# Optimization experiments

Measured on AMD Instinct MI355X. Metric: run time of the kernel, lower is better.

The kernel has to match this reference:

```python
import jax, jax.numpy as jnp
import numpy as np

N = 100000
E = 1600000
NEG_SLOPE = 0.2

def _gat_layer(x, src, dst, W, a_s, a_d, b, n):
    # GATConv (heads=1): h = xW; alpha_ij = softmax_i(leaky_relu(a_s.h_j + a_d.h_i))
    h = x @ W                                   # [N, F]
    s_src = h @ a_s                             # [N]
    s_dst = h @ a_d                             # [N]
    logits = jax.nn.leaky_relu(s_src[src] + s_dst[dst], NEG_SLOPE)  # [E]
    m = jax.ops.segment_max(logits, dst, num_segments=n)
    m = jnp.where(jnp.isfinite(m), m, 0.0)
    w = jnp.exp(logits - m[dst])
    denom = jax.ops.segment_sum(w, dst, num_segments=n)
    alpha = w / (denom[dst] + 1e-16)            # neighbor softmax per target node
    out = jax.ops.segment_sum(alpha[:, None] * h[src], dst, num_segments=n)
    return out + b

def setup_inputs() -> dict:
    key = jax.random.key(0)
    ks = jax.random.split(key, 12)
    def glorot(k, shape):
        fan = shape[0] + shape[-1] if len(shape) > 1 else shape[0]
        return jax.random.normal(k, shape, jnp.float32) * jnp.sqrt(2.0 / fan)
    x = jax.random.normal(ks[0], (N, 128), jnp.float32)
    edge_index = jax.random.randint(ks[1], (2, E), 0, N, dtype=jnp.int32)
    return {
        'x': x, 'edge_index': edge_index,
        'W1': glorot(ks[2], (128, 64)), 'a1s': glorot(ks[3], (64,)), 'a1d': glorot(ks[4], (64,)), 'b1': jnp.zeros((64,), jnp.float32),
        'W2': glorot(ks[5], (64, 64)), 'a2s': glorot(ks[6], (64,)), 'a2d': glorot(ks[7], (64,)), 'b2': jnp.zeros((64,), jnp.float32),
        'W3': glorot(ks[8], (64, 32)), 'a3s': glorot(ks[9], (32,)), 'a3d': glorot(ks[10], (32,)), 'b3': jnp.zeros((32,), jnp.float32),
    }

def reference(x, edge_index, W1, a1s, a1d, b1, W2, a2s, a2d, b2, W3, a3s, a3d, b3):
    n = x.shape[0]
    # PyG GATConv adds self-loops by default
    loops = jnp.arange(n, dtype=edge_index.dtype)
    src = jnp.concatenate([edge_index[0], loops])
    dst = jnp.concatenate([edge_index[1], loops])
    h = _gat_layer(x, src, dst, W1, a1s, a1d, b1, n)
    h = jax.nn.relu(h)  # dropout is identity in eval mode
    h = _gat_layer(h, src, dst, W2, a2s, a2d, b2, n)
    h = jax.nn.relu(h)
    h = _gat_layer(h, src, dst, W3, a3s, a3d, b3, n)
    return jax.nn.log_softmax(h, axis=1)
```

## Files before the change

kernel.cpp:

```cpp
#include <hip/hip_runtime.h>
#include <cstddef>
#include <cstdint>

#define NEG_SLOPE 0.2f

__device__ __forceinline__ unsigned short f2bf(float f) {
    unsigned int u = __float_as_uint(f);
    u = (u + 0x7fff + ((u >> 16) & 1)) >> 16;
    return (unsigned short)u;
}
__device__ __forceinline__ float bf_lo(unsigned int u) { return __uint_as_float(u << 16); }
__device__ __forceinline__ float bf_hi(unsigned int u) { return __uint_as_float(u & 0xffff0000u); }

typedef __attribute__((ext_vector_type(8))) short bf16x8;
typedef __attribute__((ext_vector_type(4))) float f32x4;
typedef __attribute__((ext_vector_type(2))) float f32x2;


constexpr int BIN_BLOCKS = 256;
constexpr int MAX_NBK = 1024;

__global__ __launch_bounds__(256) void zero_k(int* __restrict__ p, int n) {
    int i = blockIdx.x * blockDim.x + threadIdx.x;
    if (i < n) p[i] = 0;
}

__global__ __launch_bounds__(256) void bin_hist_k(const int* __restrict__ dst, int E,
                                                  int* __restrict__ btot,
                                                  int* __restrict__ blkoff,
                                                  int nbk, int chunk) {
    __shared__ int hist[MAX_NBK];
    for (int i = threadIdx.x; i < nbk; i += 256) hist[i] = 0;
    __syncthreads();
    const int lo = blockIdx.x * chunk;
    const int hi = min(lo + chunk, E);
    for (int e = lo + threadIdx.x; e < hi; e += 256)
        atomicAdd(&hist[dst[e] >> 7], 1);
    __syncthreads();
    const int B = gridDim.x;
    for (int i = threadIdx.x; i < nbk; i += 256)
        blkoff[i * B + blockIdx.x] = atomicAdd(&btot[i], hist[i]);
}

__global__ __launch_bounds__(256) void scan_small_k(const int* __restrict__ btot,
                                                    int* __restrict__ obk, int nbk) {
    __shared__ int sh[MAX_NBK];
    const int tid = threadIdx.x;
    for (int i = tid; i < nbk; i += 256) sh[i] = btot[i];
    __syncthreads();
    if (tid < 64) {
        int run = 0;
        for (int b0 = 0; b0 < nbk; b0 += 64) {
            const int i = b0 + tid;
            int v = (i < nbk) ? sh[i] : 0;
            int inc = v;
#pragma unroll
            for (int o = 1; o < 64; o <<= 1) {
                int u = __shfl_up(inc, o);
                if (tid >= o) inc += u;
            }
            if (i < nbk) sh[i] = run + inc - v;
            run += __shfl(inc, 63);
        }
        if (tid == 0) obk[nbk] = run;
    }
    __syncthreads();
    for (int i = tid; i < nbk; i += 256) obk[i] = sh[i];
}

__global__ __launch_bounds__(256) void bin_scatter_k(const int* __restrict__ ei, int E,
                                                     const int* __restrict__ obk,
                                                     const int* __restrict__ blkoff,
                                                     int* __restrict__ eb, int nbk,
                                                     int chunk) {
    __shared__ int cur[MAX_NBK];
    __shared__ int off_s[MAX_NBK];
    const int B = gridDim.x;
    for (int i = threadIdx.x; i < nbk; i += 256) {
        cur[i] = 0;
        off_s[i] = obk[i] + blkoff[i * B + blockIdx.x];
    }
    __syncthreads();
    const int lo = blockIdx.x * chunk;
    const int hi = min(lo + chunk, E);
    for (int e = lo + threadIdx.x; e < hi; e += 256) {
        int s = ei[e];
        int d = ei[E + e];
        int b = d >> 7;
        int idx = atomicAdd(&cur[b], 1);
        eb[off_s[b] + idx] = (s << 7) | (d & 127);
    }
}

__global__ __launch_bounds__(256) void bucket_build_k(const int* __restrict__ eb,
                                                      const int* __restrict__ obk,
                                                      int* __restrict__ row_ptr,
                                                      int* __restrict__ col,
                                                      int* __restrict__ edst,
                                                      int n, int nbk) {
    __shared__ int c[128];
    __shared__ int rp[128];
    const int b = blockIdx.x;
    const int t = threadIdx.x;
    const int beg = obk[b];
    const int end = obk[b + 1];
    const int bbase = beg + b * 128;
    if (t < 128) c[t] = 1;
    __syncthreads();
    for (int i = beg + t; i < end; i += 256)
        atomicAdd(&c[eb[i] & 127], 1);
    __syncthreads();
    if (t < 64) {
        int v0 = c[2 * t], v1 = c[2 * t + 1];
        int pair = v0 + v1;
        int inc = pair;
        for (int o = 1; o < 64; o <<= 1) {
            int u = __shfl_up(inc, o);
            if (t >= o) inc += u;
        }
        int ex = inc - pair;
        rp[2 * t] = bbase + ex;
        rp[2 * t + 1] = bbase + ex + v0;
    }
    __syncthreads();
    const int node = b * 128 + t;
    if (t < 128 && node < n) {
        row_ptr[node] = rp[t];
        col[rp[t]] = node;
        edst[rp[t]] = node;
    }
    if (b == 0 && t == 0) row_ptr[n] = obk[nbk] + n;
    __syncthreads();
    if (t < 128) c[t] = 1;
    __syncthreads();
    for (int i = beg + t; i < end; i += 256) {
        int p = eb[i];
        int dl = p & 127;
        int idx = atomicAdd(&c[dl], 1);
        const int slot = rp[dl] + idx;
        col[slot] = p >> 7;
        edst[slot] = b * 128 + dl;
    }
}


__global__ __launch_bounds__(256) void edge_w_k(const int* __restrict__ col,
                                                const int* __restrict__ edst,
                                                const float2* __restrict__ ssd,
                                                int2* __restrict__ ew, int EN) {
    const int e = blockIdx.x * blockDim.x + threadIdx.x;
    if (e >= EN) return;
    const int c = col[e];
    const int d = edst[e];
    const float2 pc = ssd[c];
    const float2 pd = ssd[d];
    float zs = pd.x + pd.y;
    zs = (zs > 0.f) ? zs : NEG_SLOPE * zs;
    float z = pc.x + pd.y;
    z = (z > 0.f) ? z : NEG_SLOPE * z;
    const float w = __expf(z - zs);
    ew[e] = make_int2((int)(((unsigned int)f2bf(w) << 17) | (unsigned int)c),
                      __float_as_int(w));
}


template <int K, int F>
__launch_bounds__(256)
__global__ void gemm_mfma_k(const float* __restrict__ x, const float* __restrict__ W,
                            const float* __restrict__ a_s, const float* __restrict__ a_d,
                            unsigned short* __restrict__ hb, float2* __restrict__ ssd,
                            int n) {
    constexpr int MT = 64;
    constexpr int KP = K + 8;
    constexpr int NT = F / 16;
    constexpr int KC = K / 32;

    __shared__ unsigned short xb[MT * KP];
    __shared__ unsigned short wb[F * KP];

    const int tid = threadIdx.x;
    const int lane = tid & 63;
    const int wv = tid >> 6;
    const int base = blockIdx.x * MT;

    for (int i = tid; i < MT * K / 4; i += 256) {
        int row = i / (K / 4);
        int c4 = i % (K / 4);
        float4 v = make_float4(0.f, 0.f, 0.f, 0.f);
        if (base + row < n)
            v = *(const float4*)&x[(size_t)(base + row) * K + 4 * c4];
        ushort4 b;
        b.x = f2bf(v.x); b.y = f2bf(v.y); b.z = f2bf(v.z); b.w = f2bf(v.w);
        *(ushort4*)&xb[row * KP + 4 * c4] = b;
    }
    for (int i = tid; i < K * F / 4; i += 256) {
        int nn = i % F;
        int k4 = i / F;
        ushort4 b;
        b.x = f2bf(W[(size_t)(4 * k4 + 0) * F + nn]);
        b.y = f2bf(W[(size_t)(4 * k4 + 1) * F + nn]);
        b.z = f2bf(W[(size_t)(4 * k4 + 2) * F + nn]);
        b.w = f2bf(W[(size_t)(4 * k4 + 3) * F + nn]);
        *(ushort4*)&wb[nn * KP + 4 * k4] = b;
    }
    __syncthreads();

    const int mrow = lane & 15;
    const int quad = lane >> 4;

    f32x4 acc[NT];
#pragma unroll
    for (int t = 0; t < NT; ++t) acc[t] = (f32x4){0.f, 0.f, 0.f, 0.f};

#pragma unroll
    for (int kc = 0; kc < KC; ++kc) {
        const int kof = kc * 32 + quad * 8;
        bf16x8 af = *(const bf16x8*)&xb[(wv * 16 + mrow) * KP + kof];
#pragma unroll
        for (int t = 0; t < NT; ++t) {
            bf16x8 bfr = *(const bf16x8*)&wb[(t * 16 + mrow) * KP + kof];
            acc[t] = __builtin_amdgcn_mfma_f32_16x16x32_bf16(af, bfr, acc[t], 0, 0, 0);
        }
    }

    float as_c[NT], ad_c[NT];
#pragma unroll
    for (int t = 0; t < NT; ++t) { as_c[t] = a_s[t * 16 + mrow]; ad_c[t] = a_d[t * 16 + mrow]; }

#pragma unroll
    for (int r = 0; r < 4; ++r) {
        const int node = base + wv * 16 + quad * 4 + r;
        float ps = 0.f, pd = 0.f;
#pragma unroll
        for (int t = 0; t < NT; ++t) {
            ps = fmaf(acc[t][r], as_c[t], ps);
            pd = fmaf(acc[t][r], ad_c[t], pd);
        }
#pragma unroll
        for (int o = 1; o < 16; o <<= 1) {
            ps += __shfl_xor(ps, o);
            pd += __shfl_xor(pd, o);
        }
        if (node < n) {
#pragma unroll
            for (int t = 0; t < NT; ++t)
                hb[(size_t)node * F + t * 16 + mrow] = f2bf(acc[t][r]);
            if (mrow == 0) ssd[node] = make_float2(ps, pd);
        }
    }
}


template <int K, int F>
__launch_bounds__(512)
__global__ void agg_gemm_k(const int* __restrict__ row_ptr,
                           const int2* __restrict__ ew,
                           const unsigned short* __restrict__ hbi,
                           const float* __restrict__ bias,
                           const float* __restrict__ W,
                           const float* __restrict__ a_s, const float* __restrict__ a_d,
                           unsigned short* __restrict__ hbo, float2* __restrict__ ssdo,
                           int n) {
    static_assert(K == 64, "agg phase assumes 64 input channels");
    constexpr int S = 8;
    constexpr int MT = 64;
    constexpr int KP = K + 8;
    constexpr int NT = F / 16;
    constexpr int KC = K / 32;

    __shared__ unsigned short xb[MT * KP];
    __shared__ unsigned short wb[F * KP];

    const int tid = threadIdx.x;
    const int lane = tid & 63;
    const int wv = tid >> 6;
    const int base = blockIdx.x * MT;

    for (int i = tid; i < K * F / 4; i += 512) {
        int nn = i % F;
        int k4 = i / F;
        ushort4 b;
        b.x = f2bf(W[(size_t)(4 * k4 + 0) * F + nn]);
        b.y = f2bf(W[(size_t)(4 * k4 + 1) * F + nn]);
        b.z = f2bf(W[(size_t)(4 * k4 + 2) * F + nn]);
        b.w = f2bf(W[(size_t)(4 * k4 + 3) * F + nn]);
        *(ushort4*)&wb[nn * KP + 4 * k4] = b;
    }

    const int ls = lane & (S - 1);
    const int lbase = lane - ls;
    const int nl = tid >> 3;
    const int node = base + nl;

    float val[8] = {0.f, 0.f, 0.f, 0.f, 0.f, 0.f, 0.f, 0.f};
    if (node < n) {
        const int beg = row_ptr[node];
        const int end = row_ptr[node + 1];

        float s = 0.f;
        f32x2 acc2[4];
#pragma unroll
        for (int i = 0; i < 4; ++i) acc2[i] = (f32x2){0.f, 0.f};

        int2 nxt = (beg + ls < end) ? ew[beg + ls] : make_int2(0, 0);
        for (int b0 = beg; b0 < end; b0 += S) {
            const int2 cur = nxt;
            const int jn = b0 + S + ls;
            nxt = (jn < end) ? ew[jn] : make_int2(0, 0);
            s += __int_as_float(cur.y);
            const unsigned int pk = (unsigned int)cur.x;

            auto gather = [&](int tt) {
                const unsigned int pe = (unsigned int)__shfl((int)pk, lbase + tt);
                const int ct = (int)(pe & 0x1ffffu);
                const float wt = __uint_as_float((pe >> 17) << 16);
                const uint4 hv = *(const uint4*)&hbi[(size_t)ct * K + 8 * ls];
                f32x2 p;
                p.x = bf_lo(hv.x); p.y = bf_hi(hv.x); acc2[0] += p * wt;
                p.x = bf_lo(hv.y); p.y = bf_hi(hv.y); acc2[1] += p * wt;
                p.x = bf_lo(hv.z); p.y = bf_hi(hv.z); acc2[2] += p * wt;
                p.x = bf_lo(hv.w); p.y = bf_hi(hv.w); acc2[3] += p * wt;
            };

            const int cnt = min(S, end - b0);
            if (cnt == S) {
                gather(0); gather(1); gather(2); gather(3);
                gather(4); gather(5); gather(6); gather(7);
            } else {
                int t = 0;
                for (; t + 1 < cnt; t += 2) { gather(t); gather(t + 1); }
                if (t < cnt) gather(t);
            }
        }
#pragma unroll
        for (int o = S / 2; o; o >>= 1) s += __shfl_xor(s, o);
        const float inv = 1.f / (s + 1e-16f);
        val[0] = acc2[0].x; val[1] = acc2[0].y; val[2] = acc2[1].x; val[3] = acc2[1].y;
        val[4] = acc2[2].x; val[5] = acc2[2].y; val[6] = acc2[3].x; val[7] = acc2[3].y;
#pragma unroll
        for (int i = 0; i < 8; ++i)
            val[i] = fmaxf(val[i] * inv + bias[8 * ls + i], 0.f);
    }
    {
        ushort4 p0, p1;
        p0.x = f2bf(val[0]); p0.y = f2bf(val[1]); p0.z = f2bf(val[2]); p0.w = f2bf(val[3]);
        p1.x = f2bf(val[4]); p1.y = f2bf(val[5]); p1.z = f2bf(val[6]); p1.w = f2bf(val[7]);
        *(ushort4*)&xb[nl * KP + 8 * ls] = p0;
        *(ushort4*)&xb[nl * KP + 8 * ls + 4] = p1;
    }

    __syncthreads();

    if (wv < 4) {
        const int mrow = lane & 15;
        const int quad = lane >> 4;

        f32x4 acc[NT];
#pragma unroll
        for (int t = 0; t < NT; ++t) acc[t] = (f32x4){0.f, 0.f, 0.f, 0.f};

#pragma unroll
        for (int kc = 0; kc < KC; ++kc) {
            const int kof = kc * 32 + quad * 8;
            bf16x8 af = *(const bf16x8*)&xb[(wv * 16 + mrow) * KP + kof];
#pragma unroll
            for (int t = 0; t < NT; ++t) {
                bf16x8 bfr = *(const bf16x8*)&wb[(t * 16 + mrow) * KP + kof];
                acc[t] = __builtin_amdgcn_mfma_f32_16x16x32_bf16(af, bfr, acc[t], 0, 0, 0);
            }
        }

        float as_c[NT], ad_c[NT];
#pragma unroll
        for (int t = 0; t < NT; ++t) { as_c[t] = a_s[t * 16 + mrow]; ad_c[t] = a_d[t * 16 + mrow]; }

#pragma unroll
        for (int r = 0; r < 4; ++r) {
            const int node2 = base + wv * 16 + quad * 4 + r;
            float ps = 0.f, pd = 0.f;
#pragma unroll
            for (int t = 0; t < NT; ++t) {
                ps = fmaf(acc[t][r], as_c[t], ps);
                pd = fmaf(acc[t][r], ad_c[t], pd);
            }
#pragma unroll
            for (int o = 1; o < 16; o <<= 1) {
                ps += __shfl_xor(ps, o);
                pd += __shfl_xor(pd, o);
            }
            if (node2 < n) {
#pragma unroll
                for (int t = 0; t < NT; ++t)
                    hbo[(size_t)node2 * F + t * 16 + mrow] = f2bf(acc[t][r]);
                if (mrow == 0) ssdo[node2] = make_float2(ps, pd);
            }
        }
    }
}


template <int F, int S>
__launch_bounds__(256)
__global__ void gat_agg_k(const int* __restrict__ row_ptr,
                          const int2* __restrict__ ew,
                          const unsigned short* __restrict__ hb,
                          const float* __restrict__ bias,
                          float* __restrict__ out, int n) {
    constexpr int NPW = 64 / S;
    constexpr int NL = F / 8;
    constexpr int Q = S / NL;
    const int lane = threadIdx.x & 63;
    const int ls   = lane % S;
    const int q    = ls / NL;
    const int cl   = ls % NL;
    const int lbase = lane - ls;
    const int wave = (blockIdx.x * blockDim.x + threadIdx.x) >> 6;
    const int node = wave * NPW + lane / S;
    if (node >= n) return;

    const int beg = row_ptr[node];
    const int end = row_ptr[node + 1];

    float s = 0.f;
    f32x2 acc2[4];
#pragma unroll
    for (int i = 0; i < 4; ++i) acc2[i] = (f32x2){0.f, 0.f};

    int2 nxt = (beg + ls < end) ? ew[beg + ls] : make_int2(0, 0);
    for (int b0 = beg; b0 < end; b0 += S) {
        const int2 cur = nxt;
        const int jn = b0 + S + ls;
        nxt = (jn < end) ? ew[jn] : make_int2(0, 0);
        s += __int_as_float(cur.y);
        const unsigned int pk = (unsigned int)cur.x;

        auto gather = [&](int tt) {
            const unsigned int pe = (unsigned int)__shfl((int)pk, lbase + Q * tt + q);
            const int ct = (int)(pe & 0x1ffffu);
            const float wt = __uint_as_float((pe >> 17) << 16);
            const uint4 hv = *(const uint4*)&hb[(size_t)ct * F + 8 * cl];
            f32x2 p;
            p.x = bf_lo(hv.x); p.y = bf_hi(hv.x); acc2[0] += p * wt;
            p.x = bf_lo(hv.y); p.y = bf_hi(hv.y); acc2[1] += p * wt;
            p.x = bf_lo(hv.z); p.y = bf_hi(hv.z); acc2[2] += p * wt;
            p.x = bf_lo(hv.w); p.y = bf_hi(hv.w); acc2[3] += p * wt;
        };

        const int cnt = min(S, end - b0);
        if (cnt == S) {
#pragma unroll
            for (int t = 0; t < S / Q; ++t) gather(t);
        } else {
            int t = 0;
            for (; Q * (t + 1) < cnt; t += 2) { gather(t); gather(t + 1); }
            if (Q * t < cnt) gather(t);
        }
    }

#pragma unroll
    for (int o = S / 2; o; o >>= 1) s += __shfl_xor(s, o);
    float val[8] = {acc2[0].x, acc2[0].y, acc2[1].x, acc2[1].y,
                    acc2[2].x, acc2[2].y, acc2[3].x, acc2[3].y};
#pragma unroll
    for (int o = NL; o < S; o <<= 1) {
#pragma unroll
        for (int i = 0; i < 8; ++i) val[i] += __shfl_xor(val[i], o);
    }

    const float inv = 1.f / (s + 1e-16f);
#pragma unroll
    for (int i = 0; i < 8; ++i)
        val[i] = val[i] * inv + bias[8 * cl + i];

    float lm = val[0];
#pragma unroll
    for (int i = 1; i < 8; ++i) lm = fmaxf(lm, val[i]);
#pragma unroll
    for (int o = 1; o < NL; o <<= 1) lm = fmaxf(lm, __shfl_xor(lm, o));
    float ex = 0.f;
#pragma unroll
    for (int i = 0; i < 8; ++i) ex += __expf(val[i] - lm);
#pragma unroll
    for (int o = 1; o < NL; o <<= 1) ex += __shfl_xor(ex, o);
    const float lse = lm + __logf(ex);
#pragma unroll
    for (int i = 0; i < 8; ++i) val[i] -= lse;

    if (q == 0) {
        float4 v0 = make_float4(val[0], val[1], val[2], val[3]);
        float4 v1 = make_float4(val[4], val[5], val[6], val[7]);
        *(float4*)&out[(size_t)node * F + 8 * cl] = v0;
        *(float4*)&out[(size_t)node * F + 8 * cl + 4] = v1;
    }
}


extern "C" void kernel_launch(void* const* d_in, const int* in_sizes, int n_in,
                              void* d_out, int out_size, void* d_ws, size_t ws_size,
                              hipStream_t stream) {
    const float* x  = (const float*)d_in[0];
    const int*   ei = (const int*)d_in[1];
    const float* W1 = (const float*)d_in[2];
    const float* a1s = (const float*)d_in[3];
    const float* a1d = (const float*)d_in[4];
    const float* b1  = (const float*)d_in[5];
    const float* W2 = (const float*)d_in[6];
    const float* a2s = (const float*)d_in[7];
    const float* a2d = (const float*)d_in[8];
    const float* b2  = (const float*)d_in[9];
    const float* W3 = (const float*)d_in[10];
    const float* a3s = (const float*)d_in[11];
    const float* a3d = (const float*)d_in[12];
    const float* b3  = (const float*)d_in[13];

    const int N = in_sizes[0] / 128;
    const int E = in_sizes[1] / 2;
    const int EN = E + N;
    const int NBK = (N + 127) / 128;
    const int B = BIN_BLOCKS;

    char* wp = (char*)d_ws;
    auto alloc = [&](size_t bytes) -> void* {
        void* p = wp;
        wp += (bytes + 255) & ~(size_t)255;
        return p;
    };
    int* row_ptr = (int*)alloc((size_t)(N + 1) * 4);
    int* col     = (int*)alloc((size_t)EN * 4);
    int* edst    = (int*)alloc((size_t)EN * 4);
    int2* ewb    = (int2*)alloc((size_t)EN * 8);
    unsigned short* hb1 = (unsigned short*)alloc((size_t)N * 64 * 2);
    unsigned short* hb2 = (unsigned short*)alloc((size_t)N * 64 * 2);
    unsigned short* hb3 = (unsigned short*)alloc((size_t)N * 32 * 2);
    float2* ssd1 = (float2*)alloc((size_t)N * 8);
    float2* ssd2 = (float2*)alloc((size_t)N * 8);
    float2* ssd3 = (float2*)alloc((size_t)N * 8);
    int* btot   = (int*)alloc((size_t)NBK * 4);
    int* blkoff = (int*)alloc((size_t)NBK * B * 4);
    int* obk    = (int*)alloc((size_t)(NBK + 1) * 4);
    int* eb     = (int*)alloc((size_t)E * 4);

    const int chunk = (E + B - 1) / B;

    zero_k<<<(NBK + 255) / 256, 256, 0, stream>>>(btot, NBK);
    bin_hist_k<<<B, 256, 0, stream>>>(ei + E, E, btot, blkoff, NBK, chunk);
    scan_small_k<<<1, 256, 0, stream>>>(btot, obk, NBK);
    bin_scatter_k<<<B, 256, 0, stream>>>(ei, E, obk, blkoff, eb, NBK, chunk);
    bucket_build_k<<<NBK, 256, 0, stream>>>(eb, obk, row_ptr, col, edst, N, NBK);

    const int GB = (N + 63) / 64;
    const int GE = (EN + 255) / 256;

    gemm_mfma_k<128, 64><<<GB, 256, 0, stream>>>(x, W1, a1s, a1d, hb1, ssd1, N);
    edge_w_k<<<GE, 256, 0, stream>>>(col, edst, ssd1, ewb, EN);
    agg_gemm_k<64, 64><<<GB, 512, 0, stream>>>(row_ptr, ewb, hb1, b1,
                                               W2, a2s, a2d, hb2, ssd2, N);
    edge_w_k<<<GE, 256, 0, stream>>>(col, edst, ssd2, ewb, EN);
    agg_gemm_k<64, 32><<<GB, 512, 0, stream>>>(row_ptr, ewb, hb2, b2,
                                               W3, a3s, a3d, hb3, ssd3, N);
    edge_w_k<<<GE, 256, 0, stream>>>(col, edst, ssd3, ewb, EN);
    gat_agg_k<32, 16><<<(N + 15) / 16, 256, 0, stream>>>(
        row_ptr, ewb, hb3, b3, (float*)d_out, N);
}
```

Baseline: 322.3 us.

## Fuse edge attention weight computation into aggregation kernels, drop edst and ew buffers

Removes the separate edge_w_k pass and the edst/ew arrays. Each aggregation kernel now computes the per-edge softmax weight on the fly from col and the per-node score pairs, using the self-loop logit as the stabilizer. The gather loop is restructured to issue all row loads before the FMAs, with the next batch's weight computed in between. This removes three edge-sized kernels plus their write and reread traffic, at the cost of an extra random ssd read per edge inside the aggregation.

```diff
diff --git a/kernel.cpp b/kernel.cpp
--- a/kernel.cpp
+++ b/kernel.cpp
@@ -96,7 +96,6 @@
                                                       const int* __restrict__ obk,
                                                       int* __restrict__ row_ptr,
                                                       int* __restrict__ col,
-                                                      int* __restrict__ edst,
                                                       int n, int nbk) {
     __shared__ int c[128];
     __shared__ int rp[128];
@@ -127,7 +126,6 @@
     if (t < 128 && node < n) {
         row_ptr[node] = rp[t];
         col[rp[t]] = node;
-        edst[rp[t]] = node;
     }
     if (b == 0 && t == 0) row_ptr[n] = obk[nbk] + n;
     __syncthreads();
@@ -137,30 +135,8 @@
         int p = eb[i];
         int dl = p & 127;
         int idx = atomicAdd(&c[dl], 1);
-        const int slot = rp[dl] + idx;
-        col[slot] = p >> 7;
-        edst[slot] = b * 128 + dl;
-    }
-}
-
-
-__global__ __launch_bounds__(256) void edge_w_k(const int* __restrict__ col,
-                                                const int* __restrict__ edst,
-                                                const float2* __restrict__ ssd,
-                                                int2* __restrict__ ew, int EN) {
-    const int e = blockIdx.x * blockDim.x + threadIdx.x;
-    if (e >= EN) return;
-    const int c = col[e];
-    const int d = edst[e];
-    const float2 pc = ssd[c];
-    const float2 pd = ssd[d];
-    float zs = pd.x + pd.y;
-    zs = (zs > 0.f) ? zs : NEG_SLOPE * zs;
-    float z = pc.x + pd.y;
-    z = (z > 0.f) ? z : NEG_SLOPE * z;
-    const float w = __expf(z - zs);
-    ew[e] = make_int2((int)(((unsigned int)f2bf(w) << 17) | (unsigned int)c),
-                      __float_as_int(w));
+        col[rp[dl] + idx] = p >> 7;
+    }
 }
 
 
@@ -253,9 +229,9 @@
 
 template <int K, int F>
 __launch_bounds__(512)
-__global__ void agg_gemm_k(const int* __restrict__ row_ptr,
-                           const int2* __restrict__ ew,
+__global__ void agg_gemm_k(const int* __restrict__ row_ptr, const int* __restrict__ col,
                            const unsigned short* __restrict__ hbi,
+                           const float2* __restrict__ ssdi,
                            const float* __restrict__ bias,
                            const float* __restrict__ W,
                            const float* __restrict__ a_s, const float* __restrict__ a_d,
@@ -296,41 +272,66 @@
     if (node < n) {
         const int beg = row_ptr[node];
         const int end = row_ptr[node + 1];
+        const float2 sn = ssdi[node];
+        const float sdv = sn.y;
+        float z0 = sn.x + sdv;
+        z0 = (z0 > 0.f) ? z0 : NEG_SLOPE * z0;
 
         float s = 0.f;
         f32x2 acc2[4];
 #pragma unroll
         for (int i = 0; i < 4; ++i) acc2[i] = (f32x2){0.f, 0.f};
 
-        int2 nxt = (beg + ls < end) ? ew[beg + ls] : make_int2(0, 0);
+        const int j0 = beg + ls;
+        const bool vld0 = j0 < end;
+        int c_cur = vld0 ? col[j0] : 0;
+        float w_cur = 0.f;
+        if (vld0) {
+            float z = ssdi[c_cur].x + sdv;
+            z = (z > 0.f) ? z : NEG_SLOPE * z;
+            w_cur = __expf(z - z0);
+        }
+
         for (int b0 = beg; b0 < end; b0 += S) {
-            const int2 cur = nxt;
             const int jn = b0 + S + ls;
-            nxt = (jn < end) ? ew[jn] : make_int2(0, 0);
-            s += __int_as_float(cur.y);
-            const unsigned int pk = (unsigned int)cur.x;
-
-            auto gather = [&](int tt) {
-                const unsigned int pe = (unsigned int)__shfl((int)pk, lbase + tt);
-                const int ct = (int)(pe & 0x1ffffu);
-                const float wt = __uint_as_float((pe >> 17) << 16);
-                const uint4 hv = *(const uint4*)&hbi[(size_t)ct * K + 8 * ls];
-                f32x2 p;
-                p.x = bf_lo(hv.x); p.y = bf_hi(hv.x); acc2[0] += p * wt;
-                p.x = bf_lo(hv.y); p.y = bf_hi(hv.y); acc2[1] += p * wt;
-                p.x = bf_lo(hv.z); p.y = bf_hi(hv.z); acc2[2] += p * wt;
-                p.x = bf_lo(hv.w); p.y = bf_hi(hv.w); acc2[3] += p * wt;
-            };
-
-            const int cnt = min(S, end - b0);
-            if (cnt == S) {
-                gather(0); gather(1); gather(2); gather(3);
-                gather(4); gather(5); gather(6); gather(7);
-            } else {
-                int t = 0;
-                for (; t + 1 < cnt; t += 2) { gather(t); gather(t + 1); }
-                if (t < cnt) gather(t);
-            }
+            const bool vn = jn < end;
+            const int c_next = vn ? col[jn] : 0;
+
+            s += w_cur;
+            const unsigned int pk =
+                ((unsigned int)f2bf(w_cur) << 17) | (unsigned int)c_cur;
+            const int have = min(S, end - b0);
+
+            uint4 hv[8];
+            float wt[8];
+#pragma unroll
+            for (int t = 0; t < 8; ++t) {
+                if (t < have) {
+                    const unsigned int pe = (unsigned int)__shfl((int)pk, lbase + t);
+                    wt[t] = __uint_as_float((pe >> 17) << 16);
+                    hv[t] = *(const uint4*)&hbi[(size_t)(pe & 0x1ffffu) * K + 8 * ls];
+                }
+            }
+
+            float w_next = 0.f;
+            if (vn) {
+                float z = ssdi[c_next].x + sdv;
+                z = (z > 0.f) ? z : NEG_SLOPE * z;
+                w_next = __expf(z - z0);
+            }
+
+#pragma unroll
+            for (int t = 0; t < 8; ++t) {
+                if (t < have) {
+                    f32x2 p;
+                    p.x = bf_lo(hv[t].x); p.y = bf_hi(hv[t].x); acc2[0] += p * wt[t];
+                    p.x = bf_lo(hv[t].y); p.y = bf_hi(hv[t].y); acc2[1] += p * wt[t];
+                    p.x = bf_lo(hv[t].z); p.y = bf_hi(hv[t].z); acc2[2] += p * wt[t];
+                    p.x = bf_lo(hv[t].w); p.y = bf_hi(hv[t].w); acc2[3] += p * wt[t];
+                }
+            }
+            c_cur = c_next;
+            w_cur = w_next;
         }
 #pragma unroll
         for (int o = S / 2; o; o >>= 1) s += __shfl_xor(s, o);
@@ -401,14 +402,15 @@
 
 template <int F, int S>
 __launch_bounds__(256)
-__global__ void gat_agg_k(const int* __restrict__ row_ptr,
-                          const int2* __restrict__ ew,
+__global__ void gat_agg_k(const int* __restrict__ row_ptr, const int* __restrict__ col,
                           const unsigned short* __restrict__ hb,
+                          const float2* __restrict__ ssd,
                           const float* __restrict__ bias,
                           float* __restrict__ out, int n) {
     constexpr int NPW = 64 / S;
     constexpr int NL = F / 8;
     constexpr int Q = S / NL;
+    constexpr int D = S / Q;
     const int lane = threadIdx.x & 63;
     const int ls   = lane % S;
     const int q    = ls / NL;
@@ -420,41 +422,66 @@
 
     const int beg = row_ptr[node];
     const int end = row_ptr[node + 1];
+    const float2 sn = ssd[node];
+    const float sdv = sn.y;
+    float z0 = sn.x + sdv;
+    z0 = (z0 > 0.f) ? z0 : NEG_SLOPE * z0;
 
     float s = 0.f;
     f32x2 acc2[4];
 #pragma unroll
     for (int i = 0; i < 4; ++i) acc2[i] = (f32x2){0.f, 0.f};
 
-    int2 nxt = (beg + ls < end) ? ew[beg + ls] : make_int2(0, 0);
+    const int j0 = beg + ls;
+    const bool vld0 = j0 < end;
+    int c_cur = vld0 ? col[j0] : 0;
+    float w_cur = 0.f;
+    if (vld0) {
+        float z = ssd[c_cur].x + sdv;
+        z = (z > 0.f) ? z : NEG_SLOPE * z;
+        w_cur = __expf(z - z0);
+    }
+
     for (int b0 = beg; b0 < end; b0 += S) {
-        const int2 cur = nxt;
         const int jn = b0 + S + ls;
-        nxt = (jn < end) ? ew[jn] : make_int2(0, 0);
-        s += __int_as_float(cur.y);
-        const unsigned int pk = (unsigned int)cur.x;
-
-        auto gather = [&](int tt) {
-            const unsigned int pe = (unsigned int)__shfl((int)pk, lbase + Q * tt + q);
-            const int ct = (int)(pe & 0x1ffffu);
-            const float wt = __uint_as_float((pe >> 17) << 16);
-            const uint4 hv = *(const uint4*)&hb[(size_t)ct * F + 8 * cl];
-            f32x2 p;
-            p.x = bf_lo(hv.x); p.y = bf_hi(hv.x); acc2[0] += p * wt;
-            p.x = bf_lo(hv.y); p.y = bf_hi(hv.y); acc2[1] += p * wt;
-            p.x = bf_lo(hv.z); p.y = bf_hi(hv.z); acc2[2] += p * wt;
-            p.x = bf_lo(hv.w); p.y = bf_hi(hv.w); acc2[3] += p * wt;
-        };
-
-        const int cnt = min(S, end - b0);
-        if (cnt == S) {
-#pragma unroll
-            for (int t = 0; t < S / Q; ++t) gather(t);
-        } else {
-            int t = 0;
-            for (; Q * (t + 1) < cnt; t += 2) { gather(t); gather(t + 1); }
-            if (Q * t < cnt) gather(t);
-        }
+        const bool vn = jn < end;
+        const int c_next = vn ? col[jn] : 0;
+
+        s += w_cur;
+        const unsigned int pk =
+            ((unsigned int)f2bf(w_cur) << 17) | (unsigned int)c_cur;
+        const int have = min(S, end - b0);
+
+        uint4 hv[D];
+        float wt[D];
+#pragma unroll
+        for (int t = 0; t < D; ++t) {
+            if (Q * t < have) {
+                const unsigned int pe = (unsigned int)__shfl((int)pk, lbase + Q * t + q);
+                wt[t] = __uint_as_float((pe >> 17) << 16);
+                hv[t] = *(const uint4*)&hb[(size_t)(pe & 0x1ffffu) * F + 8 * cl];
+            }
+        }
+
+        float w_next = 0.f;
+        if (vn) {
+            float z = ssd[c_next].x + sdv;
+            z = (z > 0.f) ? z : NEG_SLOPE * z;
+            w_next = __expf(z - z0);
+        }
+
+#pragma unroll
+        for (int t = 0; t < D; ++t) {
+            if (Q * t < have) {
+                f32x2 p;
+                p.x = bf_lo(hv[t].x); p.y = bf_hi(hv[t].x); acc2[0] += p * wt[t];
+                p.x = bf_lo(hv[t].y); p.y = bf_hi(hv[t].y); acc2[1] += p * wt[t];
+                p.x = bf_lo(hv[t].z); p.y = bf_hi(hv[t].z); acc2[2] += p * wt[t];
+                p.x = bf_lo(hv[t].w); p.y = bf_hi(hv[t].w); acc2[3] += p * wt[t];
+            }
+        }
+        c_cur = c_next;
+        w_cur = w_next;
     }
 
 #pragma unroll
@@ -515,7 +542,6 @@
 
     const int N = in_sizes[0] / 128;
     const int E = in_sizes[1] / 2;
-    const int EN = E + N;
     const int NBK = (N + 127) / 128;
     const int B = BIN_BLOCKS;
 
@@ -526,9 +552,7 @@
         return p;
     };
     int* row_ptr = (int*)alloc((size_t)(N + 1) * 4);
-    int* col     = (int*)alloc((size_t)EN * 4);
-    int* edst    = (int*)alloc((size_t)EN * 4);
-    int2* ewb    = (int2*)alloc((size_t)EN * 8);
+    int* col     = (int*)alloc((size_t)(E + N) * 4);
     unsigned short* hb1 = (unsigned short*)alloc((size_t)N * 64 * 2);
     unsigned short* hb2 = (unsigned short*)alloc((size_t)N * 64 * 2);
     unsigned short* hb3 = (unsigned short*)alloc((size_t)N * 32 * 2);
@@ -546,19 +570,15 @@
     bin_hist_k<<<B, 256, 0, stream>>>(ei + E, E, btot, blkoff, NBK, chunk);
     scan_small_k<<<1, 256, 0, stream>>>(btot, obk, NBK);
     bin_scatter_k<<<B, 256, 0, stream>>>(ei, E, obk, blkoff, eb, NBK, chunk);
-    bucket_build_k<<<NBK, 256, 0, stream>>>(eb, obk, row_ptr, col, edst, N, NBK);
+    bucket_build_k<<<NBK, 256, 0, stream>>>(eb, obk, row_ptr, col, N, NBK);
 
     const int GB = (N + 63) / 64;
-    const int GE = (EN + 255) / 256;
 
     gemm_mfma_k<128, 64><<<GB, 256, 0, stream>>>(x, W1, a1s, a1d, hb1, ssd1, N);
-    edge_w_k<<<GE, 256, 0, stream>>>(col, edst, ssd1, ewb, EN);
-    agg_gemm_k<64, 64><<<GB, 512, 0, stream>>>(row_ptr, ewb, hb1, b1,
+    agg_gemm_k<64, 64><<<GB, 512, 0, stream>>>(row_ptr, col, hb1, ssd1, b1,
                                                W2, a2s, a2d, hb2, ssd2, N);
-    edge_w_k<<<GE, 256, 0, stream>>>(col, edst, ssd2, ewb, EN);
-    agg_gemm_k<64, 32><<<GB, 512, 0, stream>>>(row_ptr, ewb, hb2, b2,
+    agg_gemm_k<64, 32><<<GB, 512, 0, stream>>>(row_ptr, col, hb2, ssd2, b2,
                                                W3, a3s, a3d, hb3, ssd3, N);
-    edge_w_k<<<GE, 256, 0, stream>>>(col, edst, ssd3, ewb, EN);
     gat_agg_k<32, 16><<<(N + 15) / 16, 256, 0, stream>>>(
-        row_ptr, ewb, hb3, b3, (float*)d_out, N);
-}
+        row_ptr, col, hb3, ssd3, b3, (float*)d_out, N);
+}
```

Measured after the change: 288.3 us. 10.5% less time.
